# Performance work log

Measured on AMD Instinct MI355X. Metric: run time of the kernel, lower is better.

Reference implementation:

```python
import jax, jax.numpy as jnp
import numpy as np

N, E, F_IN, H, EDIM, L, OUT = 100000, 1600000, 256, 128, 16, 3, 64


def setup_inputs() -> dict:
    key = jax.random.key(0)
    ks = jax.random.split(key, 12)
    s = lambda k, shape: jax.random.normal(k, shape, jnp.float32) * 0.05
    return dict(
        x=jax.random.normal(ks[0], (N, F_IN), jnp.float32),
        edge_index=jax.random.randint(ks[1], (2, E), 0, N, jnp.int32),
        edge_attr=jax.random.normal(ks[2], (E, EDIM), jnp.float32),
        in_w=s(ks[3], (F_IN, H)), in_b=jnp.zeros((H,), jnp.float32),
        Wk=s(ks[4], (L, H, H)), bk=jnp.zeros((L, H), jnp.float32),
        Wq=s(ks[5], (L, H, H)), bq=jnp.zeros((L, H), jnp.float32),
        Wv=s(ks[6], (L, H, H)), bv=jnp.zeros((L, H), jnp.float32),
        We=s(ks[7], (L, EDIM, H)), be=jnp.zeros((L, H), jnp.float32),
        Ws=s(ks[8], (L, H, H)), bs=jnp.zeros((L, H), jnp.float32),
        ln_g=jnp.ones((L, H), jnp.float32), ln_b=jnp.zeros((L, H), jnp.float32),
        out_w=s(ks[9], (H, OUT)),
    )


def _layernorm(x, g, b, eps=1e-5):
    mu = x.mean(-1, keepdims=True)
    var = ((x - mu) ** 2).mean(-1, keepdims=True)
    return (x - mu) * jax.lax.rsqrt(var + eps) * g + b


def reference(x, edge_index, edge_attr, in_w, in_b, Wk, bk, Wq, bq, Wv, bv,
              We, be, Ws, bs, ln_g, ln_b, out_w):
    src, dst = edge_index[0], edge_index[1]  # j (source), i (target)
    h = x @ in_w + in_b                      # in_proj; dropout_prob=0 -> identity
    n = h.shape[0]
    n_layers = Wk.shape[0]
    for l in range(n_layers):
        # ResGatedGraphConv: out_i = W_skip x_i + sum_j sigmoid(k_i + e_ij + q_j) * v_j
        k = h @ Wk[l] + bk[l]                # keys on targets  [N,H]
        q = h @ Wq[l] + bq[l]                # queries on sources [N,H]
        v = h @ Wv[l] + bv[l]                # values on sources [N,H]
        e = edge_attr @ We[l] + be[l]        # edge embedding [E,H]
        gate = jax.nn.sigmoid(k[dst] + e + q[src])   # [E,H]
        msg = gate * v[src]                  # [E,H]
        agg = jax.ops.segment_sum(msg, dst, num_segments=n)  # scatter-add [N,H]
        h = agg + (h @ Ws[l] + bs[l])        # root/skip term
        h = jax.nn.gelu(_layernorm(h, ln_g[l], ln_b[l]), approximate=False)
    return h @ out_w                          # out_proj (bias=False)
```

## Files before the change

### kernel.cpp

```cpp
#include <hip/hip_runtime.h>
#include <hip/hip_fp16.h>
#include <cmath>

#define Nn   100000
#define Ee   1600000
#define FIN  256
#define Hh   128
#define EDIMM 16
#define NL   3
#define NOUT 64
#define LOG2E 1.4426950408889634f

typedef _Float16 f16x8 __attribute__((ext_vector_type(8)));
typedef float f32x4 __attribute__((ext_vector_type(4)));

static __device__ __forceinline__ __half2 u2h2(unsigned int u) {
  union { unsigned int u; __half2 h; } c; c.u = u; return c.h;
}
static __device__ __forceinline__ unsigned int h22u(__half2 h) {
  union { unsigned int u; __half2 h; } c; c.h = h; return c.u;
}

#define PK_FMA_LO(acc, a, w) \
  asm("v_pk_fma_f16 %0, %1, %2, %0 op_sel:[0,0,0] op_sel_hi:[0,1,1]" \
      : "+v"(acc) : "v"(a), "v"(w))
#define PK_FMA_HI(acc, a, w) \
  asm("v_pk_fma_f16 %0, %1, %2, %0 op_sel:[1,0,0] op_sel_hi:[1,1,1]" \
      : "+v"(acc) : "v"(a), "v"(w))

__global__ __launch_bounds__(256) void prep_inw_kernel(const float* __restrict__ in_w,
    __half* __restrict__ in_wT) {
  int i = blockIdx.x * 256 + threadIdx.x;
  if (i < FIN * Hh) {
    int k = i >> 7, n = i & 127;
    in_wT[(size_t)n * FIN + k] = __float2half(in_w[i]);
  }
}

__global__ __launch_bounds__(256) void in_proj_mfma_kernel(const float* __restrict__ x,
    const __half* __restrict__ in_wT, const float* __restrict__ b, __half* __restrict__ h) {
  __shared__ __half Wl[128][136];
  __shared__ __half Ht[32][136];
  int r0 = blockIdx.x * 32;
  int tid = threadIdx.x;
  int wv = tid >> 6, lane = tid & 63;
  int rowHalf = wv & 1, colHalf = wv >> 1;
  int quad = lane >> 4, l16 = lane & 15;

  f32x4 acc[4];
#pragma unroll
  for (int t = 0; t < 4; t++) acc[t] = (f32x4){0.f, 0.f, 0.f, 0.f};

  for (int ph = 0; ph < 2; ph++) {
    for (int i = tid; i < 2048; i += 256) {
      int rw = i >> 4, cw = i & 15;
      *(uint4*)(&Wl[rw][cw * 8]) =
          *(const uint4*)(in_wT + (size_t)rw * FIN + ph * 128 + cw * 8);
    }
    for (int i = tid; i < 1024; i += 256) {
      int r = i >> 5, c4 = i & 31;
      float4 f = *(const float4*)(x + (size_t)(r0 + r) * FIN + ph * 128 + c4 * 4);
      *(uint2*)(&Ht[r][c4 * 4]) =
          make_uint2(h22u(__floats2half2_rn(f.x, f.y)), h22u(__floats2half2_rn(f.z, f.w)));
    }
    __syncthreads();
#pragma unroll
    for (int kstep = 0; kstep < 4; kstep++) {
      f16x8 afrag = *(const f16x8*)(&Ht[rowHalf * 16 + l16][kstep * 32 + quad * 8]);
#pragma unroll
      for (int t = 0; t < 4; t++) {
        int n = colHalf * 64 + t * 16 + l16;
        f16x8 bfrag = *(const f16x8*)(&Wl[n][kstep * 32 + quad * 8]);
        acc[t] = __builtin_amdgcn_mfma_f32_16x16x32_f16(afrag, bfrag, acc[t], 0, 0, 0);
      }
    }
    __syncthreads();
  }

#pragma unroll
  for (int t = 0; t < 4; t++) {
    int col = colHalf * 64 + t * 16 + l16;
    float bval = b[col];
#pragma unroll
    for (int r = 0; r < 4; r++) {
      int row = r0 + rowHalf * 16 + quad * 4 + r;
      h[(size_t)row * Hh + col] = __float2half(acc[t][r] + bval);
    }
  }
}

__global__ __launch_bounds__(256) void prep_weights_kernel(const float* __restrict__ Wk,
    const float* __restrict__ Wq, const float* __restrict__ Wv, const float* __restrict__ Ws,
    __half* __restrict__ WtT) {
  int mat = blockIdx.x, l = blockIdx.y;
  const float* W = (mat == 0 ? Wk : mat == 1 ? Wq : mat == 2 ? Wv : Ws) + (size_t)l * Hh * Hh;
  float sc = (mat < 2) ? LOG2E : 1.f;
  __half* out = WtT + ((size_t)(l * 4 + mat)) * Hh * Hh;
  for (int i = threadIdx.x; i < Hh * Hh; i += 256) {
    int k = i >> 7, n = i & 127;
    out[(size_t)n * Hh + k] = __float2half(W[i] * sc);
  }
}

__global__ __launch_bounds__(256) void kqvs_mfma_kernel(
    const __half* __restrict__ h, const __half* __restrict__ WtT_l,
    const float* __restrict__ bk, const float* __restrict__ bq,
    const float* __restrict__ bv, const float* __restrict__ bs,
    __half* __restrict__ kb, __half* __restrict__ qvj, __half* __restrict__ hnew) {
  __shared__ __half Wl[128][136];
  __shared__ __half Ht[32][136];
  int mat = blockIdx.x;
  int r0 = blockIdx.y * 32;
  int tid = threadIdx.x;

  const uint4* wg = (const uint4*)(WtT_l + (size_t)mat * Hh * Hh);
  for (int i = tid; i < 2048; i += 256) {
    int rw = i >> 4, cw = i & 15;
    *(uint4*)(&Wl[rw][cw * 8]) = wg[i];
  }
  const uint4* hg = (const uint4*)(h + (size_t)r0 * Hh);
  for (int i = tid; i < 512; i += 256) {
    int rh = i >> 4, ch = i & 15;
    *(uint4*)(&Ht[rh][ch * 8]) = hg[i];
  }
  __syncthreads();

  int wv = tid >> 6, lane = tid & 63;
  int rowHalf = wv & 1, colHalf = wv >> 1;
  int quad = lane >> 4, l16 = lane & 15;

  f32x4 acc[4];
#pragma unroll
  for (int t = 0; t < 4; t++) acc[t] = (f32x4){0.f, 0.f, 0.f, 0.f};

#pragma unroll
  for (int kstep = 0; kstep < 4; kstep++) {
    f16x8 afrag = *(const f16x8*)(&Ht[rowHalf * 16 + l16][kstep * 32 + quad * 8]);
#pragma unroll
    for (int t = 0; t < 4; t++) {
      int n = colHalf * 64 + t * 16 + l16;
      f16x8 bfrag = *(const f16x8*)(&Wl[n][kstep * 32 + quad * 8]);
      acc[t] = __builtin_amdgcn_mfma_f32_16x16x32_f16(afrag, bfrag, acc[t], 0, 0, 0);
    }
  }

  const float* bp = (mat == 0) ? bk : (mat == 1) ? bq : (mat == 2) ? bv : bs;
  float bscale = (mat < 2) ? LOG2E : 1.f;
#pragma unroll
  for (int t = 0; t < 4; t++) {
    int col = colHalf * 64 + t * 16 + l16;
    float bval = bp[col] * bscale;
#pragma unroll
    for (int r = 0; r < 4; r++) {
      int row = r0 + rowHalf * 16 + quad * 4 + r;
      __half hv = __float2half(acc[t][r] + bval);
      if (mat == 0)       kb[(size_t)row * Hh + col] = hv;
      else if (mat == 1)  qvj[(size_t)row * 256 + (col >> 1) * 4 + (col & 1)] = hv;
      else if (mat == 2)  qvj[(size_t)row * 256 + (col >> 1) * 4 + 2 + (col & 1)] = hv;
      else                hnew[(size_t)row * Hh + col] = hv;
    }
  }
}

__global__ __launch_bounds__(256) void zero_kernel(int* __restrict__ p, int n) {
  int i = blockIdx.x * 256 + threadIdx.x;
  if (i < n) p[i] = 0;
}

__global__ __launch_bounds__(256) void hist_kernel(const int* __restrict__ ei_dst,
                                                   int* __restrict__ counts) {
  int e = blockIdx.x * 256 + threadIdx.x;
  if (e < Ee) atomicAdd(&counts[ei_dst[e]], 1);
}

__global__ __launch_bounds__(256) void scan_block_kernel(const int* __restrict__ counts,
    int* __restrict__ rowptr, int* __restrict__ bsums) {
  __shared__ int tsums[256];
  int b = blockIdx.x, t = threadIdx.x;
  int base = b * 1024 + t * 4;
  int v[4]; int s = 0;
#pragma unroll
  for (int j = 0; j < 4; j++) {
    int idx = base + j;
    v[j] = (idx < Nn) ? counts[idx] : 0;
    s += v[j];
  }
  tsums[t] = s;
  __syncthreads();
  for (int off = 1; off < 256; off <<= 1) {
    int y = (t >= off) ? tsums[t - off] : 0;
    __syncthreads();
    tsums[t] += y;
    __syncthreads();
  }
  int excl = tsums[t] - s;
#pragma unroll
  for (int j = 0; j < 4; j++) {
    int idx = base + j;
    if (idx < Nn) rowptr[idx] = excl;
    excl += v[j];
  }
  if (t == 255) bsums[b] = tsums[255];
}

__global__ __launch_bounds__(128) void scan_sums_kernel(int* __restrict__ bsums, int nb) {
  __shared__ int sh[128];
  int t = threadIdx.x;
  int v = (t < nb) ? bsums[t] : 0;
  sh[t] = v;
  __syncthreads();
  for (int off = 1; off < 128; off <<= 1) {
    int y = (t >= off) ? sh[t - off] : 0;
    __syncthreads();
    sh[t] += y;
    __syncthreads();
  }
  if (t < nb) bsums[t] = sh[t] - v;
}

__global__ __launch_bounds__(256) void finalize_rowptr_kernel(int* __restrict__ rowptr,
    const int* __restrict__ bsums, int* __restrict__ cursor) {
  int i = blockIdx.x * 256 + threadIdx.x;
  if (i < Nn) {
    int r = rowptr[i] + bsums[i >> 10];
    rowptr[i] = r;
    cursor[i] = r;
  }
  if (i == Nn) rowptr[Nn] = Ee;
}

__global__ __launch_bounds__(256) void fill_perm_kernel(const int* __restrict__ ei_src,
    const int* __restrict__ ei_dst, const float* __restrict__ ea,
    int* __restrict__ cursor, int* __restrict__ src_perm,
    unsigned int* __restrict__ ea_perm) {
  int e = blockIdx.x * 256 + threadIdx.x;
  if (e < Ee) {
    int d = ei_dst[e];
    int slot = atomicAdd(&cursor[d], 1);
    src_perm[slot] = ei_src[e];
    const float4* s = (const float4*)(ea + (size_t)e * EDIMM);
    float4 f0 = s[0], f1 = s[1], f2 = s[2], f3 = s[3];
    uint4* dp = (uint4*)(ea_perm + (size_t)slot * 8);
    dp[0] = make_uint4(h22u(__floats2half2_rn(f0.x, f0.y)), h22u(__floats2half2_rn(f0.z, f0.w)),
                       h22u(__floats2half2_rn(f1.x, f1.y)), h22u(__floats2half2_rn(f1.z, f1.w)));
    dp[1] = make_uint4(h22u(__floats2half2_rn(f2.x, f2.y)), h22u(__floats2half2_rn(f2.z, f2.w)),
                       h22u(__floats2half2_rn(f3.x, f3.y)), h22u(__floats2half2_rn(f3.z, f3.w)));
  }
}

#define EA_CAP2 80
__global__ __launch_bounds__(256, 6) void edge_csr_kernel(
    const __half* __restrict__ kb, const __half* __restrict__ qvj,
    const int* __restrict__ src_perm, const unsigned int* __restrict__ ea_perm,
    const int* __restrict__ rowptr,
    const float* __restrict__ We_l, const float* __restrict__ be_l,
    const float* __restrict__ ln_g_l, const float* __restrict__ ln_b_l,
    __half* __restrict__ hbuf) {
  __shared__ uint4 lds_ea[4][EA_CAP2 * 2];
  int wave = threadIdx.x >> 6;
  int lane = threadIdx.x & 63;
  int r0 = (blockIdx.x * 4 + wave) * 2;
  int c0 = lane * 2;

  unsigned wpk[EDIMM];
#pragma unroll
  for (int d = 0; d < EDIMM; d++) {
    float2 wv = *(const float2*)(We_l + d * Hh + c0);
    wpk[d] = h22u(__floats2half2_rn(wv.x * LOG2E, wv.y * LOG2E));
  }
  float2 bef = *(const float2*)(be_l + c0);
  __half2 bev = __floats2half2_rn(bef.x * LOG2E, bef.y * LOG2E);

  int rpA = rowptr[r0], rpB = rowptr[r0 + 1], rpC = rowptr[r0 + 2];

  unsigned kbev0 = h22u(__hadd2(*(const __half2*)(kb + (size_t)r0 * Hh + c0), bev));
  unsigned kbev1 = h22u(__hadd2(*(const __half2*)(kb + (size_t)(r0 + 1) * Hh + c0), bev));

  int nl = rpC - rpA;
  if (nl > EA_CAP2) nl = EA_CAP2;

  char* lbase = (char*)&lds_ea[wave][0];
  {
    int row_bytes = nl << 5;
    const char* gsrc = (const char*)(ea_perm + (size_t)rpA * 8);
    for (int c = 0; c < row_bytes; c += 1024) {
      int o = c + lane * 16;
      if (o < row_bytes) {
        __builtin_amdgcn_global_load_lds(
            (__attribute__((address_space(1))) void*)(gsrc + o),
            (__attribute__((address_space(3))) void*)(lbase + c),
            16, 0, 0);
      }
    }
  }

  const char* qvb = (const char*)qvj;
  unsigned loff = (unsigned)(lane << 3);
  const int* spb = src_perm + rpA;

#pragma unroll
  for (int ri = 0; ri < 2; ri++) {
    unsigned kb_u = ri ? kbev1 : kbev0;
    float agg0 = 0.f, agg1 = 0.f;
    int ls = (ri ? rpB : rpA) - rpA;
    int le = (ri ? rpC : rpB) - rpA;
    int lend = le < nl ? le : nl;
    if (lend < ls) lend = ls;

    auto edge_math = [&](uint4 eA, uint4 eB, uint2 qv) {
      unsigned acc = kb_u;
      PK_FMA_LO(acc, eA.x, wpk[0]);  PK_FMA_HI(acc, eA.x, wpk[1]);
      PK_FMA_LO(acc, eA.y, wpk[2]);  PK_FMA_HI(acc, eA.y, wpk[3]);
      PK_FMA_LO(acc, eA.z, wpk[4]);  PK_FMA_HI(acc, eA.z, wpk[5]);
      PK_FMA_LO(acc, eA.w, wpk[6]);  PK_FMA_HI(acc, eA.w, wpk[7]);
      PK_FMA_LO(acc, eB.x, wpk[8]);  PK_FMA_HI(acc, eB.x, wpk[9]);
      PK_FMA_LO(acc, eB.y, wpk[10]); PK_FMA_HI(acc, eB.y, wpk[11]);
      PK_FMA_LO(acc, eB.z, wpk[12]); PK_FMA_HI(acc, eB.z, wpk[13]);
      PK_FMA_LO(acc, eB.w, wpk[14]); PK_FMA_HI(acc, eB.w, wpk[15]);
      __half2 pre = __hadd2(u2h2(acc), u2h2(qv.x));
      float p0 = __half2float(__low2half(pre));
      float p1 = __half2float(__high2half(pre));
      float ex0, ex1;
      asm("v_exp_f32 %0, -%1" : "=v"(ex0) : "v"(p0));
      asm("v_exp_f32 %0, -%1" : "=v"(ex1) : "v"(p1));
      float g0 = __builtin_amdgcn_rcpf(1.f + ex0);
      float g1 = __builtin_amdgcn_rcpf(1.f + ex1);
      __half2 vh = u2h2(qv.y);
      agg0 += g0 * __half2float(__low2half(vh));
      agg1 += g1 * __half2float(__high2half(vh));
    };

    int e = ls;
    int nfull = (lend - e) & ~3;
    int nfe = e + nfull;
    uint2 qA0, qA1, qA2, qA3;
    if (nfull) {
      int4 s4 = *(const int4*)(spb + e);
      qA0 = *(const uint2*)(qvb + (((unsigned)s4.x << 9) + loff));
      qA1 = *(const uint2*)(qvb + (((unsigned)s4.y << 9) + loff));
      qA2 = *(const uint2*)(qvb + (((unsigned)s4.z << 9) + loff));
      qA3 = *(const uint2*)(qvb + (((unsigned)s4.w << 9) + loff));
    }
    asm volatile("s_waitcnt vmcnt(0)" ::: "memory");

    for (; e + 8 <= nfe; e += 4) {
      int4 s4n = *(const int4*)(spb + e + 4);
      uint2 qB0 = *(const uint2*)(qvb + (((unsigned)s4n.x << 9) + loff));
      uint2 qB1 = *(const uint2*)(qvb + (((unsigned)s4n.y << 9) + loff));
      uint2 qB2 = *(const uint2*)(qvb + (((unsigned)s4n.z << 9) + loff));
      uint2 qB3 = *(const uint2*)(qvb + (((unsigned)s4n.w << 9) + loff));
      const uint4* ee = (const uint4*)(lbase + (e << 5));
      edge_math(ee[0], ee[1], qA0);
      edge_math(ee[2], ee[3], qA1);
      edge_math(ee[4], ee[5], qA2);
      edge_math(ee[6], ee[7], qA3);
      qA0 = qB0; qA1 = qB1; qA2 = qB2; qA3 = qB3;
    }
    if (nfull) {
      const uint4* ee = (const uint4*)(lbase + (e << 5));
      edge_math(ee[0], ee[1], qA0);
      edge_math(ee[2], ee[3], qA1);
      edge_math(ee[4], ee[5], qA2);
      edge_math(ee[6], ee[7], qA3);
      e += 4;
    }
    for (; e < lend; e++) {
      int src = spb[e];
      uint2 qv = *(const uint2*)(qvb + (((unsigned)src << 9) + loff));
      const uint4* ee = (const uint4*)(lbase + (e << 5));
      edge_math(ee[0], ee[1], qv);
    }
    for (int eg = rpA + lend; eg < rpA + le; eg++) {
      int src = src_perm[eg];
      const uint4* eb = (const uint4*)(ea_perm + (size_t)eg * 8);
      uint4 a0 = eb[0], a1 = eb[1];
      uint2 qv = *(const uint2*)(qvb + (((unsigned)src << 9) + loff));
      edge_math(a0, a1, qv);
    }

    int row = r0 + ri;
    __half2 hv2 = *(const __half2*)(hbuf + (size_t)row * Hh + c0);
    float y0 = __half2float(hv2.x) + agg0, y1 = __half2float(hv2.y) + agg1;
    float s = y0 + y1;
#pragma unroll
    for (int off = 32; off; off >>= 1) s += __shfl_xor(s, off);
    float mu = s * (1.f / 128.f);
    float d0 = y0 - mu, d1 = y1 - mu;
    float vv = d0 * d0 + d1 * d1;
#pragma unroll
    for (int off = 32; off; off >>= 1) vv += __shfl_xor(vv, off);
    float rstd = rsqrtf(vv * (1.f / 128.f) + 1e-5f);
    float2 lg = *(const float2*)(ln_g_l + c0);
    float2 lb = *(const float2*)(ln_b_l + c0);
    float o0 = d0 * rstd * lg.x + lb.x;
    float o1 = d1 * rstd * lg.y + lb.y;
    o0 = 0.5f * o0 * (1.f + erff(o0 * 0.70710678118654752f));
    o1 = 0.5f * o1 * (1.f + erff(o1 * 0.70710678118654752f));
    *(__half2*)(hbuf + (size_t)row * Hh + c0) = __floats2half2_rn(o0, o1);
  }
}

__global__ __launch_bounds__(64) void out_proj_kernel(const __half* __restrict__ h,
    const float* __restrict__ w, float* __restrict__ out) {
  __shared__ float hs[16][Hh];
  int r0 = blockIdx.x * 16;
  const uint4* hg = (const uint4*)(h + (size_t)r0 * Hh);
  for (int i = threadIdx.x; i < 256; i += 64) {
    uint4 u = hg[i];
    int r = i >> 4, c = (i & 15) * 8;
    __half2 ha = u2h2(u.x), hb = u2h2(u.y), hc = u2h2(u.z), hd = u2h2(u.w);
    hs[r][c+0] = __half2float(ha.x); hs[r][c+1] = __half2float(ha.y);
    hs[r][c+2] = __half2float(hb.x); hs[r][c+3] = __half2float(hb.y);
    hs[r][c+4] = __half2float(hc.x); hs[r][c+5] = __half2float(hc.y);
    hs[r][c+6] = __half2float(hd.x); hs[r][c+7] = __half2float(hd.y);
  }
  __syncthreads();
  int t = threadIdx.x;
  float acc[16] = {};
  for (int kk = 0; kk < Hh; kk++) {
    float wv = w[kk * NOUT + t];
#pragma unroll
    for (int r = 0; r < 16; r++) acc[r] += hs[r][kk] * wv;
  }
#pragma unroll
  for (int r = 0; r < 16; r++) out[(size_t)(r0 + r) * NOUT + t] = acc[r];
}

extern "C" void kernel_launch(void* const* d_in, const int* in_sizes, int n_in,
                              void* d_out, int out_size, void* d_ws, size_t ws_size,
                              hipStream_t stream) {
  const float* x    = (const float*)d_in[0];
  const int*   ei   = (const int*)d_in[1];
  const float* ea   = (const float*)d_in[2];
  const float* in_w = (const float*)d_in[3];
  const float* in_b = (const float*)d_in[4];
  const float* Wk   = (const float*)d_in[5];
  const float* bk   = (const float*)d_in[6];
  const float* Wq   = (const float*)d_in[7];
  const float* bq   = (const float*)d_in[8];
  const float* Wv   = (const float*)d_in[9];
  const float* bv   = (const float*)d_in[10];
  const float* We   = (const float*)d_in[11];
  const float* be   = (const float*)d_in[12];
  const float* Ws   = (const float*)d_in[13];
  const float* bs   = (const float*)d_in[14];
  const float* ln_g = (const float*)d_in[15];
  const float* ln_b = (const float*)d_in[16];
  const float* out_w = (const float*)d_in[17];
  float* out = (float*)d_out;

  const int* ei_src = ei;
  const int* ei_dst = ei + Ee;

  size_t NH = (size_t)Nn * Hh;
  char* wsp = (char*)d_ws;
  __half* hA = (__half*)wsp;          wsp += NH * 2;
  __half* hB = (__half*)wsp;          wsp += NH * 2;
  __half* kb = (__half*)wsp;          wsp += NH * 2;
  __half* qvj = (__half*)wsp;         wsp += NH * 2 * 2;
  __half* WtT = (__half*)wsp;         wsp += (size_t)NL * 4 * Hh * Hh * 2;
  __half* in_wT = (__half*)wsp;       wsp += (size_t)FIN * Hh * 2;
  int* rowptr = (int*)wsp;            wsp += (Nn + 1) * 4;
  int* cursor = (int*)wsp;            wsp += Nn * 4;
  int* bsums  = (int*)wsp;            wsp += 128 * 4;
  int* src_perm = (int*)wsp;          wsp += (size_t)Ee * 4;
  unsigned int* ea_perm = (unsigned int*)wsp; wsp += (size_t)Ee * 32;

  const int NB_SCAN = (Nn + 1023) / 1024;

  zero_kernel<<<(Nn + 255) / 256, 256, 0, stream>>>(cursor, Nn);
  hist_kernel<<<(Ee + 255) / 256, 256, 0, stream>>>(ei_dst, cursor);
  scan_block_kernel<<<NB_SCAN, 256, 0, stream>>>(cursor, rowptr, bsums);
  scan_sums_kernel<<<1, 128, 0, stream>>>(bsums, NB_SCAN);
  finalize_rowptr_kernel<<<(Nn + 1 + 255) / 256, 256, 0, stream>>>(rowptr, bsums, cursor);
  fill_perm_kernel<<<(Ee + 255) / 256, 256, 0, stream>>>(ei_src, ei_dst, ea, cursor,
                                                         src_perm, ea_perm);
  prep_weights_kernel<<<dim3(4, NL), 256, 0, stream>>>(Wk, Wq, Wv, Ws, WtT);
  prep_inw_kernel<<<(FIN * Hh + 255) / 256, 256, 0, stream>>>(in_w, in_wT);

  in_proj_mfma_kernel<<<Nn / 32, 256, 0, stream>>>(x, in_wT, in_b, hA);

  __half* h  = hA;
  __half* hn = hB;
  for (int l = 0; l < NL; l++) {
    kqvs_mfma_kernel<<<dim3(4, Nn / 32), 256, 0, stream>>>(h,
        WtT + (size_t)l * 4 * Hh * Hh,
        bk + l * Hh, bq + l * Hh, bv + l * Hh, bs + l * Hh,
        kb, qvj, hn);
    edge_csr_kernel<<<Nn / 8, 256, 0, stream>>>(kb, qvj, src_perm, ea_perm,
        rowptr, We + l * EDIMM * Hh, be + l * Hh,
        ln_g + l * Hh, ln_b + l * Hh, hn);
    __half* tmp = h; h = hn; hn = tmp;
  }

  out_proj_kernel<<<Nn / 16, 64, 0, stream>>>(h, out_w, out);
}
```

Measured before the change: 1.185 ms.

## Make kqvs GEMM blocks persistent over 5 row tiles with double-buffered h loads

Each block of the per-layer K/Q/V/Skip projection now handles five consecutive 32-row tiles instead of one. The 128x128 weight tile is loaded into LDS once and reused across them, and bias values are hoisted into registers. The next h tile is prefetched into registers and written into an alternate LDS buffer, so its global load overlaps the current tile's MFMA and store work. In exchange the grid shrinks from 12500 to 2500 blocks and LDS use per block grows, which may lower occupancy and latency hiding.

```diff
diff --git a/kernel.cpp b/kernel.cpp
--- a/kernel.cpp
+++ b/kernel.cpp
@@ -102,62 +102,89 @@
   }
 }
 
+#define KQVS_TPB 5
 __global__ __launch_bounds__(256) void kqvs_mfma_kernel(
     const __half* __restrict__ h, const __half* __restrict__ WtT_l,
     const float* __restrict__ bk, const float* __restrict__ bq,
     const float* __restrict__ bv, const float* __restrict__ bs,
     __half* __restrict__ kb, __half* __restrict__ qvj, __half* __restrict__ hnew) {
   __shared__ __half Wl[128][136];
-  __shared__ __half Ht[32][136];
+  __shared__ __half Ht[2][32][136];
   int mat = blockIdx.x;
-  int r0 = blockIdx.y * 32;
+  int tb = blockIdx.y * KQVS_TPB;
   int tid = threadIdx.x;
 
   const uint4* wg = (const uint4*)(WtT_l + (size_t)mat * Hh * Hh);
-  for (int i = tid; i < 2048; i += 256) {
+#pragma unroll
+  for (int j = 0; j < 8; j++) {
+    int i = tid + 256 * j;
     int rw = i >> 4, cw = i & 15;
     *(uint4*)(&Wl[rw][cw * 8]) = wg[i];
   }
-  const uint4* hg = (const uint4*)(h + (size_t)r0 * Hh);
-  for (int i = tid; i < 512; i += 256) {
-    int rh = i >> 4, ch = i & 15;
-    *(uint4*)(&Ht[rh][ch * 8]) = hg[i];
-  }
-  __syncthreads();
+  {
+    const uint4* hg = (const uint4*)(h + (size_t)tb * 32 * Hh);
+    uint4 a = hg[tid], b4 = hg[tid + 256];
+    int rh = tid >> 4, ch = tid & 15;
+    *(uint4*)(&Ht[0][rh][ch * 8]) = a;
+    int i2 = tid + 256; rh = i2 >> 4; ch = i2 & 15;
+    *(uint4*)(&Ht[0][rh][ch * 8]) = b4;
+  }
 
   int wv = tid >> 6, lane = tid & 63;
   int rowHalf = wv & 1, colHalf = wv >> 1;
   int quad = lane >> 4, l16 = lane & 15;
 
-  f32x4 acc[4];
-#pragma unroll
-  for (int t = 0; t < 4; t++) acc[t] = (f32x4){0.f, 0.f, 0.f, 0.f};
-
-#pragma unroll
-  for (int kstep = 0; kstep < 4; kstep++) {
-    f16x8 afrag = *(const f16x8*)(&Ht[rowHalf * 16 + l16][kstep * 32 + quad * 8]);
-#pragma unroll
-    for (int t = 0; t < 4; t++) {
-      int n = colHalf * 64 + t * 16 + l16;
-      f16x8 bfrag = *(const f16x8*)(&Wl[n][kstep * 32 + quad * 8]);
-      acc[t] = __builtin_amdgcn_mfma_f32_16x16x32_f16(afrag, bfrag, acc[t], 0, 0, 0);
-    }
-  }
-
   const float* bp = (mat == 0) ? bk : (mat == 1) ? bq : (mat == 2) ? bv : bs;
   float bscale = (mat < 2) ? LOG2E : 1.f;
-#pragma unroll
-  for (int t = 0; t < 4; t++) {
-    int col = colHalf * 64 + t * 16 + l16;
-    float bval = bp[col] * bscale;
-#pragma unroll
-    for (int r = 0; r < 4; r++) {
-      int row = r0 + rowHalf * 16 + quad * 4 + r;
-      __half hv = __float2half(acc[t][r] + bval);
-      if (mat == 0)       kb[(size_t)row * Hh + col] = hv;
-      else if (mat == 1)  qvj[(size_t)row * 256 + (col >> 1) * 4 + (col & 1)] = hv;
-      else if (mat == 2)  qvj[(size_t)row * 256 + (col >> 1) * 4 + 2 + (col & 1)] = hv;
-      else                hnew[(size_t)row * Hh + col] = hv;
+  float bval[4];
+#pragma unroll
+  for (int t = 0; t < 4; t++) bval[t] = bp[colHalf * 64 + t * 16 + l16] * bscale;
+
+  int cur = 0;
+#pragma unroll 1
+  for (int it = 0; it < KQVS_TPB; it++) {
+    uint4 ha, hb;
+    if (it < KQVS_TPB - 1) {
+      const uint4* hg = (const uint4*)(h + (size_t)(tb + it + 1) * 32 * Hh);
+      ha = hg[tid]; hb = hg[tid + 256];
+    }
+    __syncthreads();
+
+    f32x4 acc[4];
+#pragma unroll
+    for (int t = 0; t < 4; t++) acc[t] = (f32x4){0.f, 0.f, 0.f, 0.f};
+#pragma unroll
+    for (int kstep = 0; kstep < 4; kstep++) {
+      f16x8 afrag = *(const f16x8*)(&Ht[cur][rowHalf * 16 + l16][kstep * 32 + quad * 8]);
+#pragma unroll
+      for (int t = 0; t < 4; t++) {
+        int n = colHalf * 64 + t * 16 + l16;
+        f16x8 bfrag = *(const f16x8*)(&Wl[n][kstep * 32 + quad * 8]);
+        acc[t] = __builtin_amdgcn_mfma_f32_16x16x32_f16(afrag, bfrag, acc[t], 0, 0, 0);
+      }
+    }
+
+    int r0 = (tb + it) * 32;
+#pragma unroll
+    for (int t = 0; t < 4; t++) {
+      int col = colHalf * 64 + t * 16 + l16;
+#pragma unroll
+      for (int r = 0; r < 4; r++) {
+        int row = r0 + rowHalf * 16 + quad * 4 + r;
+        __half hv = __float2half(acc[t][r] + bval[t]);
+        if (mat == 0)       kb[(size_t)row * Hh + col] = hv;
+        else if (mat == 1)  qvj[(size_t)row * 256 + (col >> 1) * 4 + (col & 1)] = hv;
+        else if (mat == 2)  qvj[(size_t)row * 256 + (col >> 1) * 4 + 2 + (col & 1)] = hv;
+        else                hnew[(size_t)row * Hh + col] = hv;
+      }
+    }
+
+    if (it < KQVS_TPB - 1) {
+      int rh = tid >> 4, ch = tid & 15;
+      *(uint4*)(&Ht[cur ^ 1][rh][ch * 8]) = ha;
+      int i2 = tid + 256; rh = i2 >> 4; ch = i2 & 15;
+      *(uint4*)(&Ht[cur ^ 1][rh][ch * 8]) = hb;
+      cur ^= 1;
     }
   }
 }
@@ -483,7 +510,7 @@
   __half* h  = hA;
   __half* hn = hB;
   for (int l = 0; l < NL; l++) {
-    kqvs_mfma_kernel<<<dim3(4, Nn / 32), 256, 0, stream>>>(h,
+    kqvs_mfma_kernel<<<dim3(4, 625), 256, 0, stream>>>(h,
         WtT + (size_t)l * 4 * Hh * Hh,
         bk + l * Hh, bq + l * Hh, bv + l * Hh, bs + l * Hh,
         kb, qvj, hn);
```

Result: faster. 1.111 ms (-6.2%).
